# Performance work log

Measured on AMD Instinct MI355X. Metric: run time of the kernel, lower is better.

The kernel has to match this reference:

```python
import jax, jax.numpy as jnp
import numpy as np

N_USERS = 50000
N_ENTITIES = 150000
N_NODES = N_USERS + N_ENTITIES
N_EDGES = 3200000
BATCH = 4096
EPS = 1e-12  # F.normalize eps


def setup_inputs() -> dict:
    key = jax.random.key(0)
    ks = jax.random.split(key, 16)
    s = 0.1  # xavier-ish scale for small dims
    return {
        "user_w": jax.random.normal(ks[0], (N_USERS, 64), jnp.float32) * s,
        "entity_w": jax.random.normal(ks[1], (N_ENTITIES, 64), jnp.float32) * s,
        "W1a": jax.random.normal(ks[2], (64, 64), jnp.float32) * s,
        "b1a": jnp.zeros((64,), jnp.float32),
        "W2a": jax.random.normal(ks[3], (64, 64), jnp.float32) * s,
        "b2a": jnp.zeros((64,), jnp.float32),
        "W1b": jax.random.normal(ks[4], (64, 32), jnp.float32) * s,
        "b1b": jnp.zeros((32,), jnp.float32),
        "W2b": jax.random.normal(ks[5], (64, 32), jnp.float32) * s,
        "b2b": jnp.zeros((32,), jnp.float32),
        "values": jax.random.uniform(ks[6], (N_EDGES,), jnp.float32),
        "target": jax.random.randint(ks[7], (N_EDGES,), 0, N_NODES, jnp.int32),
        "neighbor": jax.random.randint(ks[8], (N_EDGES,), 0, N_NODES, jnp.int32),
        "user_ids": jax.random.randint(ks[9], (BATCH,), 0, N_USERS, jnp.int32),
        "pos_item_ids": jax.random.randint(ks[10], (BATCH,), 0, N_ENTITIES, jnp.int32),
        "neg_item_ids": jax.random.randint(ks[11], (BATCH,), 0, N_ENTITIES, jnp.int32),
    }


def _aggregate(features, target, neighbor, values):
    # msg = features[neighbor] * values[:, None]; h_neigh = index_add over target
    msg = features[neighbor] * values[:, None]  # (E, dim)
    return jax.ops.segment_sum(msg, target, num_segments=N_NODES)


def _gnn_layer(features, target, neighbor, values, W1, b1, W2, b2):
    h_neigh = _aggregate(features, target, neighbor, values)
    h = (features + h_neigh) @ W1 + b1 + (features * h_neigh) @ W2 + b2
    return jax.nn.leaky_relu(h, negative_slope=0.01)


def _l2norm(x):
    n = jnp.sqrt(jnp.sum(x * x, axis=1, keepdims=True))
    return x / jnp.maximum(n, EPS)


def reference(user_w, entity_w, W1a, b1a, W2a, b2a, W1b, b1b, W2b, b2b,
              values, target, neighbor, user_ids, pos_item_ids, neg_item_ids):
    all_embed = jnp.concatenate([user_w, entity_w], axis=0)  # (N, 64)
    ego = [all_embed]
    h1 = _l2norm(_gnn_layer(all_embed, target, neighbor, values, W1a, b1a, W2a, b2a))
    ego.append(h1)
    h2 = _l2norm(_gnn_layer(h1, target, neighbor, values, W1b, b1b, W2b, b2b))
    ego.append(h2)
    final_embed = jnp.concatenate(ego, axis=1)  # (N, 160)
    u = final_embed[user_ids]
    pos_i = final_embed[N_USERS + pos_item_ids]
    neg_i = final_embed[N_USERS + neg_item_ids]
    pos_scores = jnp.sum(u * pos_i, axis=1)
    neg_scores = jnp.sum(u * neg_i, axis=1)
    return (pos_scores, neg_scores)
```

## Files before the change

### kernel.cpp

```cpp
#include <hip/hip_runtime.h>

#define N_USERS    50000
#define N_ENTITIES 150000
#define N_NODES_C  200000
#define BATCH_C    4096
#define N_EDGES_C  3200000

#define CHUNK   7168
#define SG_SH   9
#define NSG     391
#define S2CAP   12288

typedef __attribute__((ext_vector_type(2))) _Float16 h2;
typedef __attribute__((ext_vector_type(8))) _Float16 half8;
typedef __attribute__((ext_vector_type(2))) __fp16 fp16x2_s;
typedef __attribute__((ext_vector_type(4))) float float4v;


__device__ __forceinline__ h2 u2h(unsigned u) {
    union { unsigned u; h2 h; } x; x.u = u; return x.h;
}
__device__ __forceinline__ unsigned pk2h(float a, float b) {
    union { fp16x2_s h; unsigned u; } x;
    x.h = __builtin_amdgcn_cvt_pkrtz(a, b);
    return x.u;
}
__device__ __forceinline__ float val_f32(unsigned e) {
    union { unsigned short s; _Float16 h; } x;
    x.s = (unsigned short)(e & 0x3FFFu);
    return (float)x.h;
}

#define CONVB 6250
__global__ __launch_bounds__(256) void prep_k(const float* __restrict__ uw,
                                              const float* __restrict__ ew,
                                              unsigned short* __restrict__ fb,
                                              const int* __restrict__ target,
                                              int* __restrict__ cntarr,
                                              int* __restrict__ sgtot,
                                              int n_edges, int nchunks)
{
    __shared__ int cnt[NSG];
    int bid = blockIdx.x;
    if (bid < nchunks) {
        int base = bid * CHUNK;
        int ccount = min(CHUNK, n_edges - base);
        for (int i = threadIdx.x; i < NSG; i += 256) cnt[i] = 0;
        __syncthreads();
        for (int i = threadIdx.x; i < ccount; i += 256)
            atomicAdd(&cnt[target[base + i] >> SG_SH], 1);
        __syncthreads();
        for (int i = threadIdx.x; i < NSG; i += 256) {
            cntarr[bid * NSG + i] = cnt[i];
            if (cnt[i]) atomicAdd(&sgtot[i], cnt[i]);
        }
    } else {
        int base8 = ((bid - nchunks) * 256 + threadIdx.x) * 8;
        const int split = N_USERS * 64;
        const float* src = (base8 < split) ? (uw + base8) : (ew + (base8 - split));
        float4 a = *(const float4*)src;
        float4 b = *(const float4*)(src + 4);
        uint4 o;
        o.x = pk2h(a.x, a.y);
        o.y = pk2h(a.z, a.w);
        o.z = pk2h(b.x, b.y);
        o.w = pk2h(b.z, b.w);
        *(uint4*)(fb + base8) = o;
    }
}

__global__ __launch_bounds__(512) void scan_k(const int* __restrict__ sgtot,
                                              int* __restrict__ sgoff,
                                              int* __restrict__ sgcur)
{
    __shared__ int part[512];
    int t = threadIdx.x;
    int v = (t < NSG) ? sgtot[t] : 0;
    part[t] = v;
    __syncthreads();
    for (int off = 1; off < 512; off <<= 1) {
        int w = (t >= off) ? part[t - off] : 0;
        __syncthreads();
        part[t] += w;
        __syncthreads();
    }
    if (t < NSG) { sgoff[t] = part[t] - v; sgcur[t] = part[t] - v; }
    if (t == NSG - 1) sgoff[NSG] = part[t];
}

__global__ __launch_bounds__(256) void scatter_k(
    const int* __restrict__ target, const int* __restrict__ neighbor,
    const float* __restrict__ values, const int* __restrict__ cntarr,
    int* __restrict__ sgcur, uint2* __restrict__ tmp2, int n_edges)
{
    __shared__ uint2 buf[CHUNK];
    __shared__ int cnt[NSG], off[NSG], pos[NSG], gbase[NSG];
    int c = blockIdx.x;
    int base = c * CHUNK;
    int ccount = min(CHUNK, n_edges - base);
    for (int i = threadIdx.x; i < NSG; i += 256) {
        int v = cntarr[c * NSG + i];
        cnt[i] = v;
        pos[i] = 0;
        gbase[i] = 0;
    }
    __syncthreads();
    for (int i = threadIdx.x; i < NSG; i += 256)
        if (cnt[i]) gbase[i] = atomicAdd(&sgcur[i], cnt[i]);
    if (threadIdx.x < 64) {
        int l = threadIdx.x;
        const int PER = (NSG + 63) / 64;
        int s0 = l * PER, s1 = min(s0 + PER, NSG);
        int sum = 0;
        for (int i = s0; i < s1; i++) sum += cnt[i];
        int run = sum;
        #pragma unroll
        for (int o = 1; o < 64; o <<= 1) { int v = __shfl_up(run, o); if (l >= o) run += v; }
        int excl = run - sum;
        for (int i = s0; i < s1; i++) { off[i] = excl; excl += cnt[i]; }
    }
    __syncthreads();
    for (int i = threadIdx.x; i < ccount; i += 256) {
        int t  = target[base + i];
        int sg = t >> SG_SH;
        _Float16 hv = (_Float16)values[base + i];
        unsigned short hb;
        __builtin_memcpy(&hb, &hv, 2);
        unsigned w = ((unsigned)neighbor[base + i] << 14) | (unsigned)(hb & 0x3FFFu);
        int p = off[sg] + atomicAdd(&pos[sg], 1);
        buf[p] = make_uint2(w, (unsigned)t);
    }
    __syncthreads();
    for (int i = threadIdx.x; i < ccount; i += 256) {
        uint2 ed = buf[i];
        int sg = (int)(ed.y >> SG_SH);
        tmp2[(size_t)(gbase[sg] + (i - off[sg]))] = ed;
    }
}

__global__ __launch_bounds__(512) void sort2_k(
    const uint2* __restrict__ tmp2, const int* __restrict__ sgoff,
    int* __restrict__ row_ptr, unsigned* __restrict__ edges)
{
    __shared__ unsigned sorted[S2CAP];
    __shared__ int cnt[512];
    __shared__ int cur[512];
    __shared__ int rp[513];
    int s = blockIdx.x;
    int node0 = s << SG_SH;
    int nn = min(512, N_NODES_C - node0);
    int sgstart = sgoff[s];
    int sgcnt = sgoff[s + 1] - sgstart;
    cnt[threadIdx.x] = 0;
    cur[threadIdx.x] = 0;
    __syncthreads();
    for (int e = threadIdx.x; e < sgcnt; e += 512)
        atomicAdd(&cnt[tmp2[(size_t)sgstart + e].y & 511u], 1);
    __syncthreads();
    if (threadIdx.x < 64) {
        int l = threadIdx.x;
        int s0 = l * 8;
        int vals[8];
        int sum = 0;
        for (int i = 0; i < 8; i++) { vals[i] = cnt[s0 + i]; sum += vals[i]; }
        int run = sum;
        #pragma unroll
        for (int o = 1; o < 64; o <<= 1) { int v = __shfl_up(run, o); if (l >= o) run += v; }
        int excl = run - sum;
        for (int i = 0; i < 8; i++) { rp[s0 + i] = excl; excl += vals[i]; }
        if (l == 63) rp[512] = excl;
    }
    __syncthreads();
    for (int i = threadIdx.x; i < nn; i += 512) row_ptr[node0 + i] = sgstart + rp[i];
    if (s == NSG - 1 && threadIdx.x == 0) row_ptr[N_NODES_C] = sgstart + sgcnt;
    for (int e = threadIdx.x; e < sgcnt; e += 512) {
        uint2 ed = tmp2[(size_t)sgstart + e];
        int tl = (int)(ed.y & 511u);
        int d  = rp[tl] + atomicAdd(&cur[tl], 1);
        if (d < S2CAP) sorted[d] = ed.x;
        else           edges[sgstart + d] = ed.x;
    }
    __syncthreads();
    int lim = min(sgcnt, S2CAP);
    for (int e = threadIdx.x; e < lim; e += 512)
        edges[sgstart + e] = sorted[e];
}

#define SPS 136
__global__ __launch_bounds__(512, 6) void layer1_pull_k(
    const unsigned short* __restrict__ fb,
    const int* __restrict__ row_ptr, const unsigned int* __restrict__ edges,
    const float* __restrict__ W1, const float* __restrict__ b1,
    const float* __restrict__ W2, const float* __restrict__ b2,
    _Float16* __restrict__ h1out, int n_nodes)
{
    __shared__ __align__(16) short wt[64 * SPS];
    __shared__ __align__(16) short sp[128 * SPS];
    __shared__ float sbias[64];

    for (int idx = threadIdx.x; idx < 64 * 64; idx += 512) {
        int kp = idx >> 6;
        int n  = idx & 63;
        int k0 = kp * 2, k1 = k0 + 1;
        float w0 = (k0 < 64) ? W1[k0 * 64 + n] : W2[(k0 - 64) * 64 + n];
        float w1 = (k1 < 64) ? W1[k1 * 64 + n] : W2[(k1 - 64) * 64 + n];
        *(unsigned*)&wt[n * SPS + k0] = pk2h(w0, w1);
    }
    if (threadIdx.x < 64) sbias[threadIdx.x] = b1[threadIdx.x] + b2[threadIdx.x];
    __syncthreads();

    int wv   = threadIdx.x >> 6;
    int lane = threadIdx.x & 63;
    int g    = lane >> 4;
    int q    = lane & 15;
    const uint2* fb2 = (const uint2*)fb;

    int nb0 = blockIdx.x * 128;

    for (int i = 0; i < 16; i += 4) {
        int mA = wv * 16 + i;
        int nodeBase = nb0 + mA;

        int es0 = 0, ee0 = 0, es1 = 0, ee1 = 0, es2 = 0, ee2 = 0, es3 = 0, ee3 = 0;
        if (nodeBase     < n_nodes) { es0 = row_ptr[nodeBase];     ee0 = row_ptr[nodeBase + 1]; }
        if (nodeBase + 1 < n_nodes) { es1 = row_ptr[nodeBase + 1]; ee1 = row_ptr[nodeBase + 2]; }
        if (nodeBase + 2 < n_nodes) { es2 = row_ptr[nodeBase + 2]; ee2 = row_ptr[nodeBase + 3]; }
        if (nodeBase + 3 < n_nodes) { es3 = row_ptr[nodeBase + 3]; ee3 = row_ptr[nodeBase + 4]; }

        h2 aLo0 = (h2){0, 0}, aHi0 = (h2){0, 0};
        h2 aLo1 = (h2){0, 0}, aHi1 = (h2){0, 0};
        h2 aLo2 = (h2){0, 0}, aHi2 = (h2){0, 0};
        h2 aLo3 = (h2){0, 0}, aHi3 = (h2){0, 0};

        int b0 = es0, b1c = es1, b2c = es2, b3c = es3;
        while (b0 < ee0 || b1c < ee1 || b2c < ee2 || b3c < ee3) {
            int c0 = ee0 - b0;  c0 = c0 < 0 ? 0 : (c0 > 64 ? 64 : c0);
            int c1 = ee1 - b1c; c1 = c1 < 0 ? 0 : (c1 > 64 ? 64 : c1);
            int c2 = ee2 - b2c; c2 = c2 < 0 ? 0 : (c2 > 64 ? 64 : c2);
            int c3 = ee3 - b3c; c3 = c3 < 0 ? 0 : (c3 > 64 ? 64 : c3);
            unsigned ev0 = (lane < c0) ? edges[b0 + lane]  : 0u;
            unsigned ev1 = (lane < c1) ? edges[b1c + lane] : 0u;
            unsigned ev2 = (lane < c2) ? edges[b2c + lane] : 0u;
            unsigned ev3 = (lane < c3) ? edges[b3c + lane] : 0u;
            int jm0 = (c0 + 3) >> 2;
            int jm1 = (c1 + 3) >> 2;
            int jm2 = (c2 + 3) >> 2;
            int jm3 = (c3 + 3) >> 2;
            int jm = max(max(jm0, jm1), max(jm2, jm3));
            #pragma unroll 4
            for (int j = 0; j < jm; j++) {
                unsigned w0 = (unsigned)__shfl((int)ev0, j * 4 + g);
                unsigned w1 = (unsigned)__shfl((int)ev1, j * 4 + g);
                unsigned w2 = (unsigned)__shfl((int)ev2, j * 4 + g);
                unsigned w3 = (unsigned)__shfl((int)ev3, j * 4 + g);
                uint2 d0 = fb2[(size_t)(w0 >> 14) * 16 + q];
                uint2 d1 = fb2[(size_t)(w1 >> 14) * 16 + q];
                uint2 d2 = fb2[(size_t)(w2 >> 14) * 16 + q];
                uint2 d3 = fb2[(size_t)(w3 >> 14) * 16 + q];
                unsigned vb0 = w0 & 0x3FFFu;
                unsigned vb1 = w1 & 0x3FFFu;
                unsigned vb2 = w2 & 0x3FFFu;
                unsigned vb3 = w3 & 0x3FFFu;
                h2 vv0 = u2h(vb0 | (vb0 << 16));
                h2 vv1 = u2h(vb1 | (vb1 << 16));
                h2 vv2 = u2h(vb2 | (vb2 << 16));
                h2 vv3 = u2h(vb3 | (vb3 << 16));
                aLo0 += u2h(d0.x) * vv0;  aHi0 += u2h(d0.y) * vv0;
                aLo1 += u2h(d1.x) * vv1;  aHi1 += u2h(d1.y) * vv1;
                aLo2 += u2h(d2.x) * vv2;  aHi2 += u2h(d2.y) * vv2;
                aLo3 += u2h(d3.x) * vv3;  aHi3 += u2h(d3.y) * vv3;
            }
            b0 += 64; b1c += 64; b2c += 64; b3c += 64;
        }

        float ac[4][4];
        ac[0][0] = (float)aLo0.x; ac[0][1] = (float)aLo0.y; ac[0][2] = (float)aHi0.x; ac[0][3] = (float)aHi0.y;
        ac[1][0] = (float)aLo1.x; ac[1][1] = (float)aLo1.y; ac[1][2] = (float)aHi1.x; ac[1][3] = (float)aHi1.y;
        ac[2][0] = (float)aLo2.x; ac[2][1] = (float)aLo2.y; ac[2][2] = (float)aHi2.x; ac[2][3] = (float)aHi2.y;
        ac[3][0] = (float)aLo3.x; ac[3][1] = (float)aLo3.y; ac[3][2] = (float)aHi3.x; ac[3][3] = (float)aHi3.y;
        #pragma unroll
        for (int s = 0; s < 4; s++)
            #pragma unroll
            for (int c = 0; c < 4; c++) {
                ac[s][c] += __shfl_xor(ac[s][c], 16);
                ac[s][c] += __shfl_xor(ac[s][c], 32);
            }

        int hseg = g >> 1;
        int prod = g & 1;
        int r0 = mA + (hseg << 1);
        int r1 = r0 + 1;
        int nd0 = nb0 + r0, nd1 = nb0 + r1;
        uint2 d0 = make_uint2(0u, 0u), d1 = make_uint2(0u, 0u);
        if (nd0 < n_nodes) d0 = fb2[(size_t)nd0 * 16 + q];
        if (nd1 < n_nodes) d1 = fb2[(size_t)nd1 * 16 + q];
        float a00 = hseg ? ac[2][0] : ac[0][0];
        float a01 = hseg ? ac[2][1] : ac[0][1];
        float a02 = hseg ? ac[2][2] : ac[0][2];
        float a03 = hseg ? ac[2][3] : ac[0][3];
        float a10 = hseg ? ac[3][0] : ac[1][0];
        float a11 = hseg ? ac[3][1] : ac[1][1];
        float a12 = hseg ? ac[3][2] : ac[1][2];
        float a13 = hseg ? ac[3][3] : ac[1][3];
        h2 s0l = u2h(d0.x), s0h = u2h(d0.y);
        h2 s1l = u2h(d1.x), s1h = u2h(d1.y);
        float f00 = (float)s0l.x, f01 = (float)s0l.y, f02 = (float)s0h.x, f03 = (float)s0h.y;
        float f10 = (float)s1l.x, f11 = (float)s1l.y, f12 = (float)s1h.x, f13 = (float)s1h.y;
        float x00 = prod ? f00 * a00 : f00 + a00;
        float x01 = prod ? f01 * a01 : f01 + a01;
        float x02 = prod ? f02 * a02 : f02 + a02;
        float x03 = prod ? f03 * a03 : f03 + a03;
        float x10 = prod ? f10 * a10 : f10 + a10;
        float x11 = prod ? f11 * a11 : f11 + a11;
        float x12 = prod ? f12 * a12 : f12 + a12;
        float x13 = prod ? f13 * a13 : f13 + a13;
        uint2 pk;
        pk.x = pk2h(x00, x01);
        pk.y = pk2h(x02, x03);
        *(uint2*)&sp[r0 * SPS + prod * 64 + q * 4] = pk;
        pk.x = pk2h(x10, x11);
        pk.y = pk2h(x12, x13);
        *(uint2*)&sp[r1 * SPS + prod * 64 + q * 4] = pk;
    }

    __builtin_amdgcn_wave_barrier();
    asm volatile("s_waitcnt lgkmcnt(0)" ::: "memory");
    __builtin_amdgcn_wave_barrier();

    float4v c0, c1, c2, c3;
    {
        float bv0 = sbias[q];
        float bv1 = sbias[16 + q];
        float bv2 = sbias[32 + q];
        float bv3 = sbias[48 + q];
        c0 = (float4v){bv0, bv0, bv0, bv0};
        c1 = (float4v){bv1, bv1, bv1, bv1};
        c2 = (float4v){bv2, bv2, bv2, bv2};
        c3 = (float4v){bv3, bv3, bv3, bv3};
    }
    #pragma unroll
    for (int kk = 0; kk < 4; kk++) {
        int ko = kk * 32 + g * 8;
        half8 a   = *(const half8*)&sp[(wv * 16 + q) * SPS + ko];
        half8 bb0 = *(const half8*)&wt[(q)      * SPS + ko];
        half8 bb1 = *(const half8*)&wt[(16 + q) * SPS + ko];
        half8 bb2 = *(const half8*)&wt[(32 + q) * SPS + ko];
        half8 bb3 = *(const half8*)&wt[(48 + q) * SPS + ko];
        c0 = __builtin_amdgcn_mfma_f32_16x16x32_f16(a, bb0, c0, 0, 0, 0);
        c1 = __builtin_amdgcn_mfma_f32_16x16x32_f16(a, bb1, c1, 0, 0, 0);
        c2 = __builtin_amdgcn_mfma_f32_16x16x32_f16(a, bb2, c2, 0, 0, 0);
        c3 = __builtin_amdgcn_mfma_f32_16x16x32_f16(a, bb3, c3, 0, 0, 0);
    }

    float ss[4];
    #pragma unroll
    for (int r = 0; r < 4; r++) {
        c0[r] = (c0[r] > 0.f) ? c0[r] : 0.01f * c0[r];
        c1[r] = (c1[r] > 0.f) ? c1[r] : 0.01f * c1[r];
        c2[r] = (c2[r] > 0.f) ? c2[r] : 0.01f * c2[r];
        c3[r] = (c3[r] > 0.f) ? c3[r] : 0.01f * c3[r];
        ss[r] = c0[r]*c0[r] + c1[r]*c1[r] + c2[r]*c2[r] + c3[r]*c3[r];
        #pragma unroll
        for (int mm = 1; mm < 16; mm <<= 1) ss[r] += __shfl_xor(ss[r], mm);
        ss[r] = 1.f / fmaxf(sqrtf(ss[r]), 1e-12f);
    }
    #pragma unroll
    for (int r = 0; r < 4; r++) {
        int node_r = nb0 + wv * 16 + g * 4 + r;
        if (node_r >= n_nodes) continue;
        size_t row = (size_t)node_r * 64;
        h1out[row +      q] = (_Float16)(c0[r] * ss[r]);
        h1out[row + 16 + q] = (_Float16)(c1[r] * ss[r]);
        h1out[row + 32 + q] = (_Float16)(c2[r] * ss[r]);
        h1out[row + 48 + q] = (_Float16)(c3[r] * ss[r]);
    }
}

__device__ __forceinline__ float layer2_row(
    const _Float16* __restrict__ h1,
    const int* __restrict__ row_ptr, const unsigned int* __restrict__ edges,
    const float* sW1, const float* sW2, const float* sb,
    int node, int lane)
{
    int es = row_ptr[node];
    int ee = row_ptr[node + 1];
    float g = 0.f;
    for (int base = es; base < ee; base += 64) {
        int cnt = min(64, ee - base);
        unsigned ev = (lane < cnt) ? edges[base + lane] : 0u;
        int j = 0;
        for (; j + 4 <= cnt; j += 4) {
            unsigned e0 = (unsigned)__shfl((int)ev, j);
            unsigned e1 = (unsigned)__shfl((int)ev, j + 1);
            unsigned e2 = (unsigned)__shfl((int)ev, j + 2);
            unsigned e3 = (unsigned)__shfl((int)ev, j + 3);
            float f0 = (float)h1[(size_t)(e0 >> 14) * 64 + lane];
            float f1 = (float)h1[(size_t)(e1 >> 14) * 64 + lane];
            float f2 = (float)h1[(size_t)(e2 >> 14) * 64 + lane];
            float f3 = (float)h1[(size_t)(e3 >> 14) * 64 + lane];
            g += val_f32(e0) * f0 + val_f32(e1) * f1
               + val_f32(e2) * f2 + val_f32(e3) * f3;
        }
        for (; j < cnt; j++) {
            unsigned e0 = (unsigned)__shfl((int)ev, j);
            float f0 = (float)h1[(size_t)(e0 >> 14) * 64 + lane];
            g += val_f32(e0) * f0;
        }
    }
    float f = (float)h1[(size_t)node * 64 + lane];
    float s = f + g;
    float p = f * g;
    int j = lane & 31;
    float acc = sb[j];
    #pragma unroll
    for (int k = 0; k < 64; k++) {
        float sk = __shfl(s, k);
        float pk = __shfl(p, k);
        acc += sk * sW1[k * 32 + j] + pk * sW2[k * 32 + j];
    }
    acc = (acc > 0.f) ? acc : 0.01f * acc;
    float sq = acc * acc;
    #pragma unroll
    for (int m = 1; m < 32; m <<= 1) sq += __shfl_xor(sq, m);
    return acc / fmaxf(sqrtf(sq), 1e-12f);
}

__global__ __launch_bounds__(256) void score_k(
    const float* __restrict__ uw, const float* __restrict__ ew,
    const _Float16* __restrict__ h1,
    const int* __restrict__ row_ptr, const unsigned int* __restrict__ edges,
    const float* __restrict__ W1b, const float* __restrict__ b1b,
    const float* __restrict__ W2b, const float* __restrict__ b2b,
    const int* __restrict__ uid, const int* __restrict__ pid,
    const int* __restrict__ nid, float* __restrict__ out)
{
    __shared__ float sW1[64 * 32];
    __shared__ float sW2[64 * 32];
    __shared__ float sb[32];
    for (int i = threadIdx.x; i < 64 * 32; i += 256) { sW1[i] = W1b[i]; sW2[i] = W2b[i]; }
    if (threadIdx.x < 32) sb[threadIdx.x] = b1b[threadIdx.x] + b2b[threadIdx.x];
    __syncthreads();

    int wave = threadIdx.x >> 6;
    int lane = threadIdx.x & 63;
    int i = blockIdx.x * 4 + wave;
    if (i >= BATCH_C) return;

    int un = uid[i];
    int pe = pid[i];
    int ne = nid[i];
    int pn = N_USERS + pe;
    int nn = N_USERS + ne;

    float acc01p, acc01n;
    {
        float u  = uw[(size_t)un * 64 + lane];
        float pv = ew[(size_t)pe * 64 + lane];
        float nv = ew[(size_t)ne * 64 + lane];
        acc01p = u * pv;
        acc01n = u * nv;
        float u1 = (float)h1[(size_t)un * 64 + lane];
        acc01p += u1 * (float)h1[(size_t)pn * 64 + lane];
        acc01n += u1 * (float)h1[(size_t)nn * 64 + lane];
    }

    float h2u = layer2_row(h1, row_ptr, edges, sW1, sW2, sb, un, lane);
    float h2p = layer2_row(h1, row_ptr, edges, sW1, sW2, sb, pn, lane);
    float h2n = layer2_row(h1, row_ptr, edges, sW1, sW2, sb, nn, lane);
    float p2 = h2u * h2p;
    float n2 = h2u * h2n;
    #pragma unroll
    for (int m = 1; m < 32; m <<= 1) { p2 += __shfl_xor(p2, m); n2 += __shfl_xor(n2, m); }

    #pragma unroll
    for (int m = 1; m < 64; m <<= 1) { acc01p += __shfl_xor(acc01p, m); acc01n += __shfl_xor(acc01n, m); }

    if (lane == 0) {
        out[i]           = acc01p + p2;
        out[BATCH_C + i] = acc01n + n2;
    }
}

extern "C" void kernel_launch(void* const* d_in, const int* in_sizes, int n_in,
                              void* d_out, int out_size, void* d_ws, size_t ws_size,
                              hipStream_t stream) {
    const float* uw   = (const float*)d_in[0];
    const float* ew   = (const float*)d_in[1];
    const float* W1a  = (const float*)d_in[2];
    const float* b1a  = (const float*)d_in[3];
    const float* W2a  = (const float*)d_in[4];
    const float* b2a  = (const float*)d_in[5];
    const float* W1b  = (const float*)d_in[6];
    const float* b1b  = (const float*)d_in[7];
    const float* W2b  = (const float*)d_in[8];
    const float* b2b  = (const float*)d_in[9];
    const float* values   = (const float*)d_in[10];
    const int*   target   = (const int*)d_in[11];
    const int*   neighbor = (const int*)d_in[12];
    const int*   uid  = (const int*)d_in[13];
    const int*   pid  = (const int*)d_in[14];
    const int*   nid  = (const int*)d_in[15];

    const int n_edges = in_sizes[10];

    char* ws = (char*)d_ws;
    int*  row_ptr    = (int*)ws;   ws += 801792;
    int*  cntarr     = (int*)ws;   ws += 704512;
    int*  sgtot      = (int*)ws;   ws += 4096;
    int*  sgoff      = (int*)ws;   ws += 4096;
    int*  sgcur      = (int*)ws;   ws += 4096;
    unsigned int*   edges = (unsigned int*)ws;   ws += (size_t)N_EDGES_C * 4;
    unsigned short* fb    = (unsigned short*)ws; ws += (size_t)N_NODES_C * 64 * 2;
    uint2*          tmp2  = (uint2*)ws;
    _Float16*       h1    = (_Float16*)ws;

    const int layer_blocks = (N_NODES_C + 127) / 128;
    const int nchunks      = (n_edges + CHUNK - 1) / CHUNK;

    hipMemsetAsync(sgtot, 0, (NSG + 1) * sizeof(int), stream);

    prep_k<<<nchunks + CONVB, 256, 0, stream>>>(uw, ew, fb, target,
                                                cntarr, sgtot, n_edges, nchunks);

    scan_k<<<1, 512, 0, stream>>>(sgtot, sgoff, sgcur);
    scatter_k<<<nchunks, 256, 0, stream>>>(target, neighbor, values, cntarr, sgcur, tmp2, n_edges);
    sort2_k<<<NSG, 512, 0, stream>>>(tmp2, sgoff, row_ptr, edges);

    layer1_pull_k<<<layer_blocks, 512, 0, stream>>>(fb, row_ptr, edges,
                                                    W1a, b1a, W2a, b2a, h1, N_NODES_C);

    score_k<<<BATCH_C / 4, 256, 0, stream>>>(uw, ew, h1, row_ptr, edges,
                                             W1b, b1b, W2b, b2b,
                                             uid, pid, nid, (float*)d_out);
}
```

Measured before the change: 328.3 us.

## Fold scan into scatter/sort kernels and batch three layer-2 rows per wave

Removes the single-block scan kernel launch by having every scatter_k and sort2_k block recompute the supergroup prefix sum from sgtot in shared memory, with sgcur now zeroed by the widened memset and used as a relative cursor. In score_k the three layer-2 row computations are interleaved so their gathers overlap, and the 64x32 matvec is split across wave halves, which halves the shuffle loop length. Costs are redundant scans in every block and lockstep iteration over the longest of the three neighbor lists.

Result: faster. 314.9 us (-4.1%).

```diff
diff --git a/kernel.cpp b/kernel.cpp
--- a/kernel.cpp
+++ b/kernel.cpp
@@ -69,57 +69,46 @@
     }
 }
 
-__global__ __launch_bounds__(512) void scan_k(const int* __restrict__ sgtot,
-                                              int* __restrict__ sgoff,
-                                              int* __restrict__ sgcur)
-{
-    __shared__ int part[512];
-    int t = threadIdx.x;
-    int v = (t < NSG) ? sgtot[t] : 0;
-    part[t] = v;
-    __syncthreads();
-    for (int off = 1; off < 512; off <<= 1) {
-        int w = (t >= off) ? part[t - off] : 0;
-        __syncthreads();
-        part[t] += w;
-        __syncthreads();
-    }
-    if (t < NSG) { sgoff[t] = part[t] - v; sgcur[t] = part[t] - v; }
-    if (t == NSG - 1) sgoff[NSG] = part[t];
-}
-
 __global__ __launch_bounds__(256) void scatter_k(
     const int* __restrict__ target, const int* __restrict__ neighbor,
     const float* __restrict__ values, const int* __restrict__ cntarr,
-    int* __restrict__ sgcur, uint2* __restrict__ tmp2, int n_edges)
+    const int* __restrict__ sgtot, int* __restrict__ sgcur,
+    uint2* __restrict__ tmp2, int n_edges)
 {
     __shared__ uint2 buf[CHUNK];
     __shared__ int cnt[NSG], off[NSG], pos[NSG], gbase[NSG];
+    __shared__ int stot[NSG], soff[NSG];
     int c = blockIdx.x;
     int base = c * CHUNK;
     int ccount = min(CHUNK, n_edges - base);
     for (int i = threadIdx.x; i < NSG; i += 256) {
-        int v = cntarr[c * NSG + i];
-        cnt[i] = v;
+        cnt[i]  = cntarr[c * NSG + i];
+        stot[i] = sgtot[i];
         pos[i] = 0;
-        gbase[i] = 0;
-    }
-    __syncthreads();
-    for (int i = threadIdx.x; i < NSG; i += 256)
-        if (cnt[i]) gbase[i] = atomicAdd(&sgcur[i], cnt[i]);
+    }
+    __syncthreads();
     if (threadIdx.x < 64) {
         int l = threadIdx.x;
         const int PER = (NSG + 63) / 64;
         int s0 = l * PER, s1 = min(s0 + PER, NSG);
         int sum = 0;
-        for (int i = s0; i < s1; i++) sum += cnt[i];
+        for (int i = s0; i < s1; i++) sum += stot[i];
         int run = sum;
         #pragma unroll
         for (int o = 1; o < 64; o <<= 1) { int v = __shfl_up(run, o); if (l >= o) run += v; }
         int excl = run - sum;
+        for (int i = s0; i < s1; i++) { soff[i] = excl; excl += stot[i]; }
+        sum = 0;
+        for (int i = s0; i < s1; i++) sum += cnt[i];
+        run = sum;
+        #pragma unroll
+        for (int o = 1; o < 64; o <<= 1) { int v = __shfl_up(run, o); if (l >= o) run += v; }
+        excl = run - sum;
         for (int i = s0; i < s1; i++) { off[i] = excl; excl += cnt[i]; }
     }
     __syncthreads();
+    for (int i = threadIdx.x; i < NSG; i += 256)
+        gbase[i] = cnt[i] ? soff[i] + atomicAdd(&sgcur[i], cnt[i]) : 0;
     for (int i = threadIdx.x; i < ccount; i += 256) {
         int t  = target[base + i];
         int sg = t >> SG_SH;
@@ -139,21 +128,36 @@
 }
 
 __global__ __launch_bounds__(512) void sort2_k(
-    const uint2* __restrict__ tmp2, const int* __restrict__ sgoff,
+    const uint2* __restrict__ tmp2, const int* __restrict__ sgtot,
     int* __restrict__ row_ptr, unsigned* __restrict__ edges)
 {
     __shared__ unsigned sorted[S2CAP];
     __shared__ int cnt[512];
     __shared__ int cur[512];
     __shared__ int rp[513];
+    __shared__ int stot[NSG], soff[NSG];
     int s = blockIdx.x;
     int node0 = s << SG_SH;
     int nn = min(512, N_NODES_C - node0);
-    int sgstart = sgoff[s];
-    int sgcnt = sgoff[s + 1] - sgstart;
     cnt[threadIdx.x] = 0;
     cur[threadIdx.x] = 0;
-    __syncthreads();
+    for (int i = threadIdx.x; i < NSG; i += 512) stot[i] = sgtot[i];
+    __syncthreads();
+    if (threadIdx.x < 64) {
+        int l = threadIdx.x;
+        const int PER = (NSG + 63) / 64;
+        int s0 = l * PER, s1 = min(s0 + PER, NSG);
+        int sum = 0;
+        for (int i = s0; i < s1; i++) sum += stot[i];
+        int run = sum;
+        #pragma unroll
+        for (int o = 1; o < 64; o <<= 1) { int v = __shfl_up(run, o); if (l >= o) run += v; }
+        int excl = run - sum;
+        for (int i = s0; i < s1; i++) { soff[i] = excl; excl += stot[i]; }
+    }
+    __syncthreads();
+    int sgstart = soff[s];
+    int sgcnt   = stot[s];
     for (int e = threadIdx.x; e < sgcnt; e += 512)
         atomicAdd(&cnt[tmp2[(size_t)sgstart + e].y & 511u], 1);
     __syncthreads();
@@ -376,53 +380,75 @@
     }
 }
 
-__device__ __forceinline__ float layer2_row(
+__device__ __forceinline__ void layer2_rows3(
     const _Float16* __restrict__ h1,
     const int* __restrict__ row_ptr, const unsigned int* __restrict__ edges,
     const float* sW1, const float* sW2, const float* sb,
-    int node, int lane)
+    int n0, int n1, int n2, int lane,
+    float& r0, float& r1, float& r2)
 {
-    int es = row_ptr[node];
-    int ee = row_ptr[node + 1];
-    float g = 0.f;
-    for (int base = es; base < ee; base += 64) {
-        int cnt = min(64, ee - base);
-        unsigned ev = (lane < cnt) ? edges[base + lane] : 0u;
-        int j = 0;
-        for (; j + 4 <= cnt; j += 4) {
-            unsigned e0 = (unsigned)__shfl((int)ev, j);
-            unsigned e1 = (unsigned)__shfl((int)ev, j + 1);
-            unsigned e2 = (unsigned)__shfl((int)ev, j + 2);
-            unsigned e3 = (unsigned)__shfl((int)ev, j + 3);
+    int es0 = row_ptr[n0], ee0 = row_ptr[n0 + 1];
+    int es1 = row_ptr[n1], ee1 = row_ptr[n1 + 1];
+    int es2 = row_ptr[n2], ee2 = row_ptr[n2 + 1];
+    float g0 = 0.f, g1 = 0.f, g2 = 0.f;
+    int b0 = es0, b1 = es1, b2 = es2;
+    while (b0 < ee0 || b1 < ee1 || b2 < ee2) {
+        int c0 = ee0 - b0; c0 = c0 < 0 ? 0 : (c0 > 64 ? 64 : c0);
+        int c1 = ee1 - b1; c1 = c1 < 0 ? 0 : (c1 > 64 ? 64 : c1);
+        int c2 = ee2 - b2; c2 = c2 < 0 ? 0 : (c2 > 64 ? 64 : c2);
+        unsigned ev0 = (lane < c0) ? edges[b0 + lane] : 0u;
+        unsigned ev1 = (lane < c1) ? edges[b1 + lane] : 0u;
+        unsigned ev2 = (lane < c2) ? edges[b2 + lane] : 0u;
+        int jm = max(c0, max(c1, c2));
+        for (int j = 0; j < jm; j++) {
+            unsigned e0 = (unsigned)__shfl((int)ev0, j);
+            unsigned e1 = (unsigned)__shfl((int)ev1, j);
+            unsigned e2 = (unsigned)__shfl((int)ev2, j);
             float f0 = (float)h1[(size_t)(e0 >> 14) * 64 + lane];
             float f1 = (float)h1[(size_t)(e1 >> 14) * 64 + lane];
             float f2 = (float)h1[(size_t)(e2 >> 14) * 64 + lane];
-            float f3 = (float)h1[(size_t)(e3 >> 14) * 64 + lane];
-            g += val_f32(e0) * f0 + val_f32(e1) * f1
-               + val_f32(e2) * f2 + val_f32(e3) * f3;
+            g0 += val_f32(e0) * f0;
+            g1 += val_f32(e1) * f1;
+            g2 += val_f32(e2) * f2;
         }
-        for (; j < cnt; j++) {
-            unsigned e0 = (unsigned)__shfl((int)ev, j);
-            float f0 = (float)h1[(size_t)(e0 >> 14) * 64 + lane];
-            g += val_f32(e0) * f0;
-        }
-    }
-    float f = (float)h1[(size_t)node * 64 + lane];
-    float s = f + g;
-    float p = f * g;
-    int j = lane & 31;
-    float acc = sb[j];
-    #pragma unroll
-    for (int k = 0; k < 64; k++) {
-        float sk = __shfl(s, k);
-        float pk = __shfl(p, k);
-        acc += sk * sW1[k * 32 + j] + pk * sW2[k * 32 + j];
-    }
-    acc = (acc > 0.f) ? acc : 0.01f * acc;
-    float sq = acc * acc;
-    #pragma unroll
-    for (int m = 1; m < 32; m <<= 1) sq += __shfl_xor(sq, m);
-    return acc / fmaxf(sqrtf(sq), 1e-12f);
+        b0 += 64; b1 += 64; b2 += 64;
+    }
+    float fA = (float)h1[(size_t)n0 * 64 + lane];
+    float fB = (float)h1[(size_t)n1 * 64 + lane];
+    float fC = (float)h1[(size_t)n2 * 64 + lane];
+    float sA = fA + g0, pA = fA * g0;
+    float sB = fB + g1, pB = fB * g1;
+    float sC = fC + g2, pC = fC * g2;
+    int j  = lane & 31;
+    int kb = (lane >> 5) << 5;
+    float aA = 0.f, aB = 0.f, aC = 0.f;
+    #pragma unroll
+    for (int k = 0; k < 32; k++) {
+        int kk = kb + k;
+        float w1v = sW1[kk * 32 + j];
+        float w2v = sW2[kk * 32 + j];
+        aA += __shfl(sA, kk) * w1v + __shfl(pA, kk) * w2v;
+        aB += __shfl(sB, kk) * w1v + __shfl(pB, kk) * w2v;
+        aC += __shfl(sC, kk) * w1v + __shfl(pC, kk) * w2v;
+    }
+    aA += __shfl_xor(aA, 32);
+    aB += __shfl_xor(aB, 32);
+    aC += __shfl_xor(aC, 32);
+    float bj = sb[j];
+    aA += bj; aB += bj; aC += bj;
+    aA = (aA > 0.f) ? aA : 0.01f * aA;
+    aB = (aB > 0.f) ? aB : 0.01f * aB;
+    aC = (aC > 0.f) ? aC : 0.01f * aC;
+    float qA = aA * aA, qB = aB * aB, qC = aC * aC;
+    #pragma unroll
+    for (int m = 1; m < 32; m <<= 1) {
+        qA += __shfl_xor(qA, m);
+        qB += __shfl_xor(qB, m);
+        qC += __shfl_xor(qC, m);
+    }
+    r0 = aA / fmaxf(sqrtf(qA), 1e-12f);
+    r1 = aB / fmaxf(sqrtf(qB), 1e-12f);
+    r2 = aC / fmaxf(sqrtf(qC), 1e-12f);
 }
 
 __global__ __launch_bounds__(256) void score_k(
@@ -464,9 +490,8 @@
         acc01n += u1 * (float)h1[(size_t)nn * 64 + lane];
     }
 
-    float h2u = layer2_row(h1, row_ptr, edges, sW1, sW2, sb, un, lane);
-    float h2p = layer2_row(h1, row_ptr, edges, sW1, sW2, sb, pn, lane);
-    float h2n = layer2_row(h1, row_ptr, edges, sW1, sW2, sb, nn, lane);
+    float h2u, h2p, h2n;
+    layer2_rows3(h1, row_ptr, edges, sW1, sW2, sb, un, pn, nn, lane, h2u, h2p, h2n);
     float p2 = h2u * h2p;
     float n2 = h2u * h2n;
     #pragma unroll
@@ -507,7 +532,6 @@
     int*  row_ptr    = (int*)ws;   ws += 801792;
     int*  cntarr     = (int*)ws;   ws += 704512;
     int*  sgtot      = (int*)ws;   ws += 4096;
-    int*  sgoff      = (int*)ws;   ws += 4096;
     int*  sgcur      = (int*)ws;   ws += 4096;
     unsigned int*   edges = (unsigned int*)ws;   ws += (size_t)N_EDGES_C * 4;
     unsigned short* fb    = (unsigned short*)ws; ws += (size_t)N_NODES_C * 64 * 2;
@@ -517,14 +541,14 @@
     const int layer_blocks = (N_NODES_C + 127) / 128;
     const int nchunks      = (n_edges + CHUNK - 1) / CHUNK;
 
-    hipMemsetAsync(sgtot, 0, (NSG + 1) * sizeof(int), stream);
+    hipMemsetAsync(sgtot, 0, 8192, stream);
 
     prep_k<<<nchunks + CONVB, 256, 0, stream>>>(uw, ew, fb, target,
                                                 cntarr, sgtot, n_edges, nchunks);
 
-    scan_k<<<1, 512, 0, stream>>>(sgtot, sgoff, sgcur);
-    scatter_k<<<nchunks, 256, 0, stream>>>(target, neighbor, values, cntarr, sgcur, tmp2, n_edges);
-    sort2_k<<<NSG, 512, 0, stream>>>(tmp2, sgoff, row_ptr, edges);
+    scatter_k<<<nchunks, 256, 0, stream>>>(target, neighbor, values, cntarr,
+                                           sgtot, sgcur, tmp2, n_edges);
+    sort2_k<<<NSG, 512, 0, stream>>>(tmp2, sgtot, row_ptr, edges);
 
     layer1_pull_k<<<layer_blocks, 512, 0, stream>>>(fb, row_ptr, edges,
                                                     W1a, b1a, W2a, b2a, h1, N_NODES_C);
```
